# Optimization experiments

Hardware: AMD Instinct MI355X
Metric: run time of the kernel (lower is better)

## Reference

```python
import jax, jax.numpy as jnp
import numpy as np

B, N, F, T, K, FO = 16, 1024, 64, 24, 3, 64


def setup_inputs() -> dict:
    key = jax.random.key(0)
    ks = jax.random.split(key, 8)
    sc = 0.05
    x = jax.random.normal(ks[0], (B, N, F, T), dtype=jnp.float32)
    W1 = jax.random.normal(ks[1], (T,), dtype=jnp.float32) * sc
    W2 = jax.random.normal(ks[2], (F, T), dtype=jnp.float32) * sc
    W3 = jax.random.normal(ks[3], (F,), dtype=jnp.float32) * sc
    bs = jax.random.normal(ks[4], (1, N, N), dtype=jnp.float32) * sc
    Vs = jax.random.normal(ks[5], (N, N), dtype=jnp.float32) * sc
    cheb = jax.random.normal(ks[6], (K, N, N), dtype=jnp.float32) * sc
    Theta = jax.random.normal(ks[7], (K, F, FO), dtype=jnp.float32) * sc
    return {"x": x, "W1": W1, "W2": W2, "W3": W3, "bs": bs, "Vs": Vs,
            "cheb": cheb, "Theta": Theta}


def spatial_attention(x, W1, W2, W3, bs, Vs):
    # x: (B,N,F,T) -> S: (B,N,N)
    lhs = jnp.einsum('bnft,t->bnf', x, W1)          # (B,N,F)
    lhs = jnp.einsum('bnf,ft->bnt', lhs, W2)        # (B,N,T)
    rhs = jnp.einsum('f,bnft->btn', W3, x)          # (B,T,N)
    product = jnp.einsum('bnt,btm->bnm', lhs, rhs)  # (B,N,N)
    S = jnp.einsum('ik,bkj->bij', Vs, jax.nn.sigmoid(product + bs))
    return jax.nn.softmax(S, axis=1)


def reference(x, W1, W2, W3, bs, Vs, cheb, Theta):
    # x: (B,N,F,T); cheb: (K,N,N); Theta: (K,F,FO)
    S = spatial_attention(x, W1, W2, W3, bs, Vs)    # (B,N,N)
    out = jnp.zeros((x.shape[0], x.shape[1], Theta.shape[2], x.shape[3]),
                    dtype=x.dtype)
    for k in range(cheb.shape[0]):                  # small fixed K
        Tat = cheb[k] * S                           # (B,N,N) attention-masked T_k
        # T_k_with_at.permute(0,2,1) @ graph_signal, vectorized over t
        r = jnp.einsum('bnm,bnft->bmft', Tat, x)    # (B,N,F,T)
        out = out + jnp.einsum('bmft,fo->bmot', r, Theta[k])
    return jax.nn.relu(out)                         # (B,N,FO,T)
```

## Files before the change

### kernel.cpp

```cpp
#include <hip/hip_runtime.h>
#include <math.h>

#define Bc 16
#define Nc 1024
#define Fc 64
#define Tc 24
#define Kc 3
#define FOc 64
#define Cc (Fc*Tc)
#define KKc (Kc*Nc)

typedef __attribute__((ext_vector_type(8))) short short8;
typedef __attribute__((ext_vector_type(4))) float f32x4;

__device__ __forceinline__ unsigned short f2bf(float f) {
  unsigned u = __float_as_uint(f);
  u += 0x7fff + ((u >> 16) & 1);
  return (unsigned short)(u >> 16);
}
__device__ __forceinline__ float bf2f(unsigned short h) {
  return __uint_as_float((unsigned)h << 16);
}

#define GLL16(g, l) __builtin_amdgcn_global_load_lds( \
    (const __attribute__((address_space(1))) void*)(g), \
    (__attribute__((address_space(3))) void*)(l), 16, 0, 0)

__device__ __forceinline__ f32x4 mfma16(short8 a, short8 b, f32x4 c) {
  return __builtin_amdgcn_mfma_f32_16x16x32_bf16(a, b, c, 0, 0, 0);
}

__device__ __forceinline__ void gemm_core(
    const unsigned short* __restrict__ Ag, const unsigned short* __restrict__ Bg,
    int lda, int ldb, int K,
    unsigned short* As, unsigned short* Bs,
    int wave, int lane, f32x4 acc[4][4]) {
  int sr = lane >> 3;
  int sc = ((lane & 7) ^ sr) * 8;
  const unsigned short* a0 = Ag + (size_t)(wave * 32 + sr) * lda + sc;
  const unsigned short* b0 = Bg + (size_t)(wave * 32 + sr) * ldb + sc;
  unsigned short* asw = As + (wave * 32) * 64;
  unsigned short* bsw = Bs + (wave * 32) * 64;
  int rw = (wave >> 1) * 64, cw = (wave & 1) * 64;
  int frow = lane & 15;
  int q = lane >> 4;
  int p0 = (q ^ (frow & 7)) * 8;
  int p1 = ((q | 4) ^ (frow & 7)) * 8;
  for (int k0 = 0; k0 < K; k0 += 64) {
    #pragma unroll
    for (int c = 0; c < 4; ++c) {
      GLL16(a0 + (size_t)(c * 8) * lda + k0, asw + (c * 8) * 64);
      GLL16(b0 + (size_t)(c * 8) * ldb + k0, bsw + (c * 8) * 64);
    }
    __syncthreads();
    #pragma unroll
    for (int h = 0; h < 2; ++h) {
      int p = h ? p1 : p0;
      short8 afr[4], bfr[4];
      #pragma unroll
      for (int i = 0; i < 4; ++i)
        afr[i] = *(const short8*)&As[(rw + i * 16 + frow) * 64 + p];
      #pragma unroll
      for (int j = 0; j < 4; ++j)
        bfr[j] = *(const short8*)&Bs[(cw + j * 16 + frow) * 64 + p];
      #pragma unroll
      for (int i = 0; i < 4; ++i)
        #pragma unroll
        for (int j = 0; j < 4; ++j)
          acc[i][j] = mfma16(afr[i], bfr[j], acc[i][j]);
    }
    __syncthreads();
  }
}

template <int MODE, int JN>
__global__ __launch_bounds__(512) void gemm256(
    const unsigned short* __restrict__ A, const unsigned short* __restrict__ B,
    void* __restrict__ Cv, int K, int CN,
    long long Abatch, long long Bbatch, long long Cbatch) {
  __shared__ unsigned short S[2 * (256 + JN * 64) * 64];
  const int BN  = JN * 64;
  const int BUF = (256 + BN) * 64;

  int gx = gridDim.x, gy = gridDim.y;
  int nwg = gx * gy * gridDim.z;
  int bid = blockIdx.x + gx * (blockIdx.y + gy * blockIdx.z);
  int xcd = bid & 7, idx = bid >> 3;
  int qq = nwg >> 3, rr = nwg & 7;
  int lin = (xcd < rr ? xcd * (qq + 1) : rr * (qq + 1) + (xcd - rr) * qq) + idx;
  int b = lin / (gx * gy);
  int rem = lin - b * (gx * gy);
  int by = rem / gx, bx = rem - by * gx;

  int tid = threadIdx.x, wave = tid >> 6, lane = tid & 63;
  const unsigned short* Ag = A + (size_t)b * Abatch + (size_t)by * 256 * K;
  const unsigned short* Bg = B + (size_t)b * Bbatch + (size_t)bx * BN * K;

  int sr = lane >> 3;
  int sc = ((lane & 7) ^ sr) * 8;
  const unsigned short* a0 = Ag + (size_t)(wave * 32 + sr) * K + sc;
  const unsigned short* b0 = Bg + (size_t)(wave * 32 + sr) * K + sc;
  unsigned short* asw0 = S + wave * 32 * 64;
  unsigned short* bsw0 = S + 256 * 64 + wave * 32 * 64;
  unsigned short* asw1 = asw0 + BUF;
  unsigned short* bsw1 = bsw0 + BUF;

  int wm = wave >> 2, wn = wave & 3;
  int rw = wm * 128;
  int cw = wn * (JN * 16);
  int frow = lane & 15;
  int q = lane >> 4;
  int p0 = (q ^ (frow & 7)) * 8;
  int p1 = ((q | 4) ^ (frow & 7)) * 8;

  f32x4 zero = {0.f, 0.f, 0.f, 0.f};
  f32x4 acc[8][JN];
  #pragma unroll
  for (int i = 0; i < 8; ++i)
    #pragma unroll
    for (int j = 0; j < JN; ++j) acc[i][j] = zero;

  auto STAGE = [&](unsigned short* asw, unsigned short* bsw, int k0) {
    #pragma unroll
    for (int c = 0; c < 4; ++c)
      GLL16(a0 + (size_t)(c * 8) * K + k0, asw + (c * 8) * 64);
    if (wave < 2 * JN) {
      #pragma unroll
      for (int c = 0; c < 4; ++c)
        GLL16(b0 + (size_t)(c * 8) * K + k0, bsw + (c * 8) * 64);
    }
  };
  auto COMPUTE = [&](const unsigned short* As, const unsigned short* Bs) {
    #pragma unroll
    for (int h = 0; h < 2; ++h) {
      int p = h ? p1 : p0;
      short8 afr[8], bfr[JN];
      #pragma unroll
      for (int i = 0; i < 8; ++i)
        afr[i] = *(const short8*)&As[(rw + i * 16 + frow) * 64 + p];
      #pragma unroll
      for (int j = 0; j < JN; ++j)
        bfr[j] = *(const short8*)&Bs[(cw + j * 16 + frow) * 64 + p];
      #pragma unroll
      for (int i = 0; i < 8; ++i)
        #pragma unroll
        for (int j = 0; j < JN; ++j)
          acc[i][j] = mfma16(afr[i], bfr[j], acc[i][j]);
    }
  };

  STAGE(asw0, bsw0, 0);
  __syncthreads();
  int k0 = 0;
  for (;;) {
    if (k0 + 64 < K) STAGE(asw1, bsw1, k0 + 64);
    COMPUTE(S, S + 256 * 64);
    __syncthreads();
    k0 += 64;
    if (k0 >= K) break;
    if (k0 + 64 < K) STAGE(asw0, bsw0, k0 + 64);
    COMPUTE(S + BUF, S + BUF + 256 * 64);
    __syncthreads();
    k0 += 64;
    if (k0 >= K) break;
  }

  int cl = lane & 15;
  #pragma unroll
  for (int i = 0; i < 8; ++i)
    #pragma unroll
    for (int e = 0; e < 4; ++e) {
      size_t P = (size_t)by * 256 + rw + i * 16 + q * 4 + e;
      #pragma unroll
      for (int j = 0; j < JN; ++j) {
        size_t Q = (size_t)bx * BN + cw + j * 16 + cl;
        if (MODE == 0) {
          ((unsigned short*)Cv)[(size_t)b * Cbatch + P * CN + Q] = f2bf(acc[i][j][e]);
        } else {
          ((float*)Cv)[(size_t)b * Cbatch + P * CN + Q] = fmaxf(acc[i][j][e], 0.f);
        }
      }
    }
}

__global__ __launch_bounds__(256) void xprep_kernel(
    const float* __restrict__ x, const float* __restrict__ W1,
    const float* __restrict__ W2, const float* __restrict__ W3,
    unsigned short* __restrict__ xt2, unsigned short* __restrict__ lhsb,
    unsigned short* __restrict__ rhsb) {
  __shared__ float ld[4 * 1560];
  __shared__ float af[4 * 64];
  int w = threadIdx.x >> 6, lane = threadIdx.x & 63;
  size_t n = (size_t)blockIdx.x * 4 + w;
  const float* xp = x + n * Cc;
  float* lw = ld + w * 1560;
  #pragma unroll
  for (int j = 0; j < 24; ++j) {
    int i = j * 64 + lane;
    int f = i / 24, t = i - f * 24;
    lw[t * 65 + f] = xp[i];
  }
  __syncthreads();
  float a = 0.f;
  #pragma unroll
  for (int t = 0; t < Tc; ++t) a += lw[t * 65 + lane] * W1[t];
  af[w * 64 + lane] = a;
  #pragma unroll
  for (int j = 0; j < 24; ++j)
    xt2[n * Cc + j * 64 + lane] = f2bf(lw[j * 65 + lane]);
  __syncthreads();
  float l = 0.f, r = 0.f;
  if (lane < Tc) {
    #pragma unroll 8
    for (int f = 0; f < Fc; ++f) {
      l += af[w * 64 + f] * W2[f * Tc + lane];
      r += W3[f] * lw[lane * 65 + f];
    }
  }
  lhsb[n * 64 + lane] = (lane < Tc) ? f2bf(l) : (unsigned short)0;
  rhsb[n * 64 + lane] = (lane < Tc) ? f2bf(r) : (unsigned short)0;
}

__global__ __launch_bounds__(256) void misc_kernel(
    const float* __restrict__ Vs, const float* __restrict__ Theta,
    const float* __restrict__ bs, unsigned short* __restrict__ Vsbf,
    unsigned short* __restrict__ tcat, float* __restrict__ bsT) {
  __shared__ float t[64 * 65];
  int bid = blockIdx.x, tid = threadIdx.x;
  if (bid < 1024) {
    int i = (bid * 256 + tid) * 4;
    float4 v = *(const float4*)&Vs[i];
    ushort4 o;
    o.x = f2bf(v.x); o.y = f2bf(v.y); o.z = f2bf(v.z); o.w = f2bf(v.w);
    *(ushort4*)&Vsbf[i] = o;
  } else if (bid < 1088) {
    int i = (bid - 1024) * 256 + tid;
    int m2 = i >> 6, f = i & 63;
    int k = m2 >> 6, o = m2 & 63;
    tcat[i] = (m2 < 192) ? f2bf(Theta[((size_t)k * Fc + f) * FOc + o])
                         : (unsigned short)0;
  } else {
    int id = bid - 1088;
    int p0 = (id >> 4) * 64, q0 = (id & 15) * 64;
    #pragma unroll
    for (int s = 0; s < 4; ++s) {
      int qr = (tid >> 4) + s * 16, pc = (tid & 15) * 4;
      float4 v = *(const float4*)&bs[(size_t)(q0 + qr) * Nc + p0 + pc];
      t[(pc + 0) * 65 + qr] = v.x;
      t[(pc + 1) * 65 + qr] = v.y;
      t[(pc + 2) * 65 + qr] = v.z;
      t[(pc + 3) * 65 + qr] = v.w;
    }
    __syncthreads();
    #pragma unroll
    for (int s = 0; s < 4; ++s) {
      int pr = (tid >> 4) + s * 16, qc = (tid & 15) * 4;
      float4 v = {t[pr * 65 + qc], t[pr * 65 + qc + 1],
                  t[pr * 65 + qc + 2], t[pr * 65 + qc + 3]};
      *(float4*)&bsT[(size_t)(p0 + pr) * Nc + q0 + qc] = v;
    }
  }
}

__global__ __launch_bounds__(256) void chebT_kernel(
    const float* __restrict__ cheb, float* __restrict__ chebT) {
  int k = blockIdx.z;
  int n0 = blockIdx.y * 64, m0 = blockIdx.x * 64;
  __shared__ float t[64 * 65];
  const float* src = cheb + (size_t)k * Nc * Nc;
  float* dst = chebT + (size_t)k * Nc * Nc;
  int tid = threadIdx.x;
  #pragma unroll
  for (int s = 0; s < 4; ++s) {
    int nr = (tid >> 4) + s * 16, mc = (tid & 15) * 4;
    float4 v = *(const float4*)&src[(size_t)(n0 + nr) * Nc + m0 + mc];
    t[(mc + 0) * 65 + nr] = v.x;
    t[(mc + 1) * 65 + nr] = v.y;
    t[(mc + 2) * 65 + nr] = v.z;
    t[(mc + 3) * 65 + nr] = v.w;
  }
  __syncthreads();
  #pragma unroll
  for (int s = 0; s < 4; ++s) {
    int mr = (tid >> 4) + s * 16, nc = (tid & 15) * 4;
    float4 v = {t[mr * 65 + nc], t[mr * 65 + nc + 1], t[mr * 65 + nc + 2], t[mr * 65 + nc + 3]};
    *(float4*)&dst[(size_t)(m0 + mr) * Nc + n0 + nc] = v;
  }
}

__global__ __launch_bounds__(256) void masksoft_kernel(
    const float* __restrict__ chebT, const unsigned short* __restrict__ ST,
    unsigned short* __restrict__ Acat, int bbase) {
  int m  = blockIdx.x & (Nc - 1);
  int bl = blockIdx.x >> 10;
  int tid = threadIdx.x;
  const unsigned short* sp = ST + ((size_t)(bbase + bl) * Nc + m) * Nc;
  ushort4 s4 = *(const ushort4*)(sp + tid * 4);
  float v0 = bf2f(s4.x), v1 = bf2f(s4.y), v2 = bf2f(s4.z), v3 = bf2f(s4.w);
  __shared__ float redm[4], reds[4];
  int wave = tid >> 6, lane = tid & 63;
  float mx = fmaxf(fmaxf(v0, v1), fmaxf(v2, v3));
  #pragma unroll
  for (int off = 32; off; off >>= 1) mx = fmaxf(mx, __shfl_xor(mx, off));
  if (lane == 0) redm[wave] = mx;
  __syncthreads();
  mx = fmaxf(fmaxf(redm[0], redm[1]), fmaxf(redm[2], redm[3]));
  float e0 = __expf(v0 - mx), e1 = __expf(v1 - mx);
  float e2 = __expf(v2 - mx), e3 = __expf(v3 - mx);
  float sm = e0 + e1 + e2 + e3;
  #pragma unroll
  for (int off = 32; off; off >>= 1) sm += __shfl_xor(sm, off);
  if (lane == 0) reds[wave] = sm;
  __syncthreads();
  float inv = 1.f / (reds[0] + reds[1] + reds[2] + reds[3]);
  e0 *= inv; e1 *= inv; e2 *= inv; e3 *= inv;
  unsigned short* ap = Acat + ((size_t)bl * Nc + m) * KKc + tid * 4;
  #pragma unroll
  for (int k = 0; k < Kc; ++k) {
    float4 c = *(const float4*)&chebT[((size_t)k * Nc + m) * Nc + tid * 4];
    ushort4 o;
    o.x = f2bf(c.x * e0); o.y = f2bf(c.y * e1);
    o.z = f2bf(c.z * e2); o.w = f2bf(c.w * e3);
    *(ushort4*)(ap + k * Nc) = o;
  }
}

template <int MODE>
__global__ __launch_bounds__(256) void mfma_gemm_bt(
    const unsigned short* __restrict__ A, const unsigned short* __restrict__ B,
    void* __restrict__ Cv, const float* __restrict__ bias, int K, int CN,
    long long Abatch, long long Bbatch, long long Cbatch) {
  __shared__ unsigned short As[128 * 64];
  __shared__ unsigned short Bs[128 * 64];
  int gx = gridDim.x, gy = gridDim.y;
  int nwg = gx * gy * gridDim.z;
  int bid = blockIdx.x + gx * (blockIdx.y + gy * blockIdx.z);
  int xcd = bid & 7, idx = bid >> 3;
  int qq = nwg >> 3, rr = nwg & 7;
  int lin = (xcd < rr ? xcd * (qq + 1) : rr * (qq + 1) + (xcd - rr) * qq) + idx;
  int b = lin / (gx * gy);
  int rem = lin - b * (gx * gy);
  int by = rem / gx, bx = rem - by * gx;
  int tid = threadIdx.x, wave = tid >> 6, lane = tid & 63;
  const unsigned short* Ag = A + (size_t)b * Abatch + (size_t)by * 128 * K;
  const unsigned short* Bg = B + (size_t)b * Bbatch + (size_t)bx * 128 * K;
  f32x4 zero = {0.f, 0.f, 0.f, 0.f};
  f32x4 acc[4][4];
  #pragma unroll
  for (int i = 0; i < 4; ++i)
    #pragma unroll
    for (int j = 0; j < 4; ++j) acc[i][j] = zero;
  gemm_core(Ag, Bg, K, K, K, As, Bs, wave, lane, acc);
  int rw = (wave >> 1) * 64, cw = (wave & 1) * 64;
  int q = lane >> 4, cl = lane & 15;
  #pragma unroll
  for (int i = 0; i < 4; ++i)
    #pragma unroll
    for (int e = 0; e < 4; ++e) {
      size_t P = (size_t)by * 128 + rw + i * 16 + q * 4 + e;
      #pragma unroll
      for (int j = 0; j < 4; ++j) {
        size_t Q = (size_t)bx * 128 + cw + j * 16 + cl;
        if (MODE == 0) {
          ((unsigned short*)Cv)[(size_t)b * Cbatch + P * CN + Q] = f2bf(acc[i][j][e]);
        } else if (MODE == 1) {
          ((float*)Cv)[(size_t)b * Cbatch + P * CN + Q] = fmaxf(acc[i][j][e], 0.f);
        } else {
          float v = acc[i][j][e] + bias[P * CN + Q];
          ((unsigned short*)Cv)[(size_t)b * Cbatch + P * CN + Q] =
              f2bf(1.f / (1.f + __expf(-v)));
        }
      }
    }
}

__global__ __launch_bounds__(256) void y2_gemm(
    const unsigned short* __restrict__ tcat, const unsigned short* __restrict__ xt2,
    unsigned short* __restrict__ ycat, int bbase) {
  __shared__ unsigned short As[128 * 64];
  __shared__ unsigned short Bs[128 * 64];
  int z = blockIdx.z;
  int bl = z / 24, t = z - bl * 24;
  int tid = threadIdx.x, wave = tid >> 6, lane = tid & 63;
  const unsigned short* Ag = tcat + (size_t)blockIdx.y * 128 * 64;
  const unsigned short* Bg = xt2 + ((size_t)(bbase + bl) * Nc + (size_t)blockIdx.x * 128) * Cc
                             + (size_t)t * 64;
  f32x4 zero = {0.f, 0.f, 0.f, 0.f};
  f32x4 acc[4][4];
  #pragma unroll
  for (int i = 0; i < 4; ++i)
    #pragma unroll
    for (int j = 0; j < 4; ++j) acc[i][j] = zero;
  gemm_core(Ag, Bg, 64, Cc, 64, As, Bs, wave, lane, acc);
  int rw = (wave >> 1) * 64, cw = (wave & 1) * 64;
  int q = lane >> 4, cl = lane & 15;
  unsigned short* yb = ycat + (size_t)bl * Cc * KKc + (size_t)t * KKc;
  #pragma unroll
  for (int i = 0; i < 4; ++i)
    #pragma unroll
    for (int e = 0; e < 4; ++e) {
      int m2 = blockIdx.y * 128 + rw + i * 16 + q * 4 + e;
      if (m2 < 192) {
        int kk = m2 >> 6, o = m2 & 63;
        unsigned short* dst = yb + (size_t)o * 24 * KKc + kk * Nc;
        #pragma unroll
        for (int j = 0; j < 4; ++j)
          dst[blockIdx.x * 128 + cw + j * 16 + cl] = f2bf(acc[i][j][e]);
      }
    }
}

extern "C" void kernel_launch(void* const* d_in, const int* in_sizes, int n_in,
                              void* d_out, int out_size, void* d_ws, size_t ws_size,
                              hipStream_t stream) {
  const float* x     = (const float*)d_in[0];
  const float* W1    = (const float*)d_in[1];
  const float* W2    = (const float*)d_in[2];
  const float* W3    = (const float*)d_in[3];
  const float* bs    = (const float*)d_in[4];
  const float* Vs    = (const float*)d_in[5];
  const float* cheb  = (const float*)d_in[6];
  const float* Theta = (const float*)d_in[7];
  float* out = (float*)d_out;

  int passes, blcount;
  if (ws_size >= 348160000ULL) { passes = 1; blcount = 16; }
  else                         { passes = 2; blcount = 8;  }

  char* w = (char*)d_ws;
  size_t Y  = (size_t)blcount * Cc * KKc * 2;
  size_t A2 = (size_t)blcount * Nc * KKc * 2;
  unsigned short* ycat = (unsigned short*)w;
  unsigned short* Acat = (unsigned short*)(w + Y);
  unsigned short* ST   = (unsigned short*)(w + Y + A2);
  float* chebT         = (float*)(w + Y + A2 + 33554432);
  unsigned short* xt2  = (unsigned short*)(w + Y + A2 + 46137344);
  unsigned short* tcat = (unsigned short*)(w + Y + A2 + 96468992);
  unsigned short* lhsb = (unsigned short*)w;
  unsigned short* rhsb = (unsigned short*)(w + 2097152);
  unsigned short* sigT = (unsigned short*)(w + 4194304);
  float* bsT           = (float*)(w + 37748736);
  unsigned short* Vsbf = (unsigned short*)(w + 41943040);

  xprep_kernel<<<Bc * Nc / 4, 256, 0, stream>>>(x, W1, W2, W3, xt2, lhsb, rhsb);
  misc_kernel<<<1344, 256, 0, stream>>>(Vs, Theta, bs, Vsbf, tcat, bsT);
  mfma_gemm_bt<2><<<dim3(8, 8, 16), 256, 0, stream>>>(
      rhsb, lhsb, sigT, bsT, 64, Nc,
      (long long)Nc * 64, (long long)Nc * 64, (long long)Nc * Nc);
  gemm256<0, 4><<<dim3(4, 4, 16), 512, 0, stream>>>(
      sigT, Vsbf, ST, Nc, Nc,
      (long long)Nc * Nc, 0LL, (long long)Nc * Nc);
  chebT_kernel<<<dim3(16, 16, 3), 256, 0, stream>>>(cheb, chebT);

  for (int pass = 0; pass < passes; ++pass) {
    int bbase = pass * blcount;
    masksoft_kernel<<<blcount * Nc, 256, 0, stream>>>(chebT, ST, Acat, bbase);
    y2_gemm<<<dim3(Nc / 128, 2, blcount * 24), 256, 0, stream>>>(tcat, xt2, ycat, bbase);
    gemm256<1, 3><<<dim3(Cc / 192, Nc / 256, blcount), 512, 0, stream>>>(
        Acat, ycat, out + (size_t)bbase * Nc * Cc, KKc, Cc,
        (long long)Nc * KKc, (long long)Cc * KKc, (long long)Nc * Cc);
  }
}
```

Measured before the change: 577.1 us.

## Replace 256-row GEMM with 128x128 triple-buffered pipelined GEMM

```diff
diff --git a/kernel.cpp b/kernel.cpp
--- a/kernel.cpp
+++ b/kernel.cpp
@@ -73,15 +73,12 @@
   }
 }
 
-template <int MODE, int JN>
-__global__ __launch_bounds__(512) void gemm256(
+template <int MODE>
+__global__ __launch_bounds__(512) void gemm_pipe(
     const unsigned short* __restrict__ A, const unsigned short* __restrict__ B,
     void* __restrict__ Cv, int K, int CN,
     long long Abatch, long long Bbatch, long long Cbatch) {
-  __shared__ unsigned short S[2 * (256 + JN * 64) * 64];
-  const int BN  = JN * 64;
-  const int BUF = (256 + BN) * 64;
-
+  __shared__ unsigned short S[6 * 128 * 64];
   int gx = gridDim.x, gy = gridDim.y;
   int nwg = gx * gy * gridDim.z;
   int bid = blockIdx.x + gx * (blockIdx.y + gy * blockIdx.z);
@@ -93,87 +90,98 @@
   int by = rem / gx, bx = rem - by * gx;
 
   int tid = threadIdx.x, wave = tid >> 6, lane = tid & 63;
-  const unsigned short* Ag = A + (size_t)b * Abatch + (size_t)by * 256 * K;
-  const unsigned short* Bg = B + (size_t)b * Bbatch + (size_t)bx * BN * K;
+  const unsigned short* Ag = A + (size_t)b * Abatch + (size_t)by * 128 * K;
+  const unsigned short* Bg = B + (size_t)b * Bbatch + (size_t)bx * 128 * K;
 
   int sr = lane >> 3;
   int sc = ((lane & 7) ^ sr) * 8;
-  const unsigned short* a0 = Ag + (size_t)(wave * 32 + sr) * K + sc;
-  const unsigned short* b0 = Bg + (size_t)(wave * 32 + sr) * K + sc;
-  unsigned short* asw0 = S + wave * 32 * 64;
-  unsigned short* bsw0 = S + 256 * 64 + wave * 32 * 64;
-  unsigned short* asw1 = asw0 + BUF;
-  unsigned short* bsw1 = bsw0 + BUF;
+  const unsigned short* a0 = Ag + (size_t)(wave * 16 + sr) * K + sc;
+  const unsigned short* b0 = Bg + (size_t)(wave * 16 + sr) * K + sc;
+  int soff = wave * 16 * 64;
+
+  unsigned short* A0 = S;
+  unsigned short* B0 = S + 128 * 64;
+  unsigned short* A1 = S + 2 * 128 * 64;
+  unsigned short* B1 = S + 3 * 128 * 64;
+  unsigned short* A2 = S + 4 * 128 * 64;
+  unsigned short* B2 = S + 5 * 128 * 64;
 
   int wm = wave >> 2, wn = wave & 3;
-  int rw = wm * 128;
-  int cw = wn * (JN * 16);
+  int rw = wm * 64, cw = wn * 32;
   int frow = lane & 15;
   int q = lane >> 4;
   int p0 = (q ^ (frow & 7)) * 8;
   int p1 = ((q | 4) ^ (frow & 7)) * 8;
 
   f32x4 zero = {0.f, 0.f, 0.f, 0.f};
-  f32x4 acc[8][JN];
-  #pragma unroll
-  for (int i = 0; i < 8; ++i)
-    #pragma unroll
-    for (int j = 0; j < JN; ++j) acc[i][j] = zero;
-
-  auto STAGE = [&](unsigned short* asw, unsigned short* bsw, int k0) {
-    #pragma unroll
-    for (int c = 0; c < 4; ++c)
-      GLL16(a0 + (size_t)(c * 8) * K + k0, asw + (c * 8) * 64);
-    if (wave < 2 * JN) {
-      #pragma unroll
-      for (int c = 0; c < 4; ++c)
-        GLL16(b0 + (size_t)(c * 8) * K + k0, bsw + (c * 8) * 64);
-    }
+  f32x4 acc[4][2];
+  #pragma unroll
+  for (int i = 0; i < 4; ++i)
+    #pragma unroll
+    for (int j = 0; j < 2; ++j) acc[i][j] = zero;
+
+  auto STAGE = [&](unsigned short* Ab, unsigned short* Bb, int k0) {
+    GLL16(a0 + k0, Ab + soff);
+    GLL16(a0 + (size_t)8 * K + k0, Ab + soff + 8 * 64);
+    GLL16(b0 + k0, Bb + soff);
+    GLL16(b0 + (size_t)8 * K + k0, Bb + soff + 8 * 64);
   };
-  auto COMPUTE = [&](const unsigned short* As, const unsigned short* Bs) {
+  auto COMPUTE = [&](const unsigned short* As_, const unsigned short* Bs_) {
     #pragma unroll
     for (int h = 0; h < 2; ++h) {
       int p = h ? p1 : p0;
-      short8 afr[8], bfr[JN];
-      #pragma unroll
-      for (int i = 0; i < 8; ++i)
-        afr[i] = *(const short8*)&As[(rw + i * 16 + frow) * 64 + p];
-      #pragma unroll
-      for (int j = 0; j < JN; ++j)
-        bfr[j] = *(const short8*)&Bs[(cw + j * 16 + frow) * 64 + p];
-      #pragma unroll
-      for (int i = 0; i < 8; ++i)
+      short8 afr[4], bfr[2];
+      #pragma unroll
+      for (int i = 0; i < 4; ++i)
+        afr[i] = *(const short8*)&As_[(rw + i * 16 + frow) * 64 + p];
+      #pragma unroll
+      for (int j = 0; j < 2; ++j)
+        bfr[j] = *(const short8*)&Bs_[(cw + j * 16 + frow) * 64 + p];
+      __builtin_amdgcn_s_setprio(1);
+      #pragma unroll
+      for (int i = 0; i < 4; ++i)
         #pragma unroll
-        for (int j = 0; j < JN; ++j)
+        for (int j = 0; j < 2; ++j)
           acc[i][j] = mfma16(afr[i], bfr[j], acc[i][j]);
+      __builtin_amdgcn_s_setprio(0);
     }
   };
 
-  STAGE(asw0, bsw0, 0);
-  __syncthreads();
-  int k0 = 0;
-  for (;;) {
-    if (k0 + 64 < K) STAGE(asw1, bsw1, k0 + 64);
-    COMPUTE(S, S + 256 * 64);
-    __syncthreads();
-    k0 += 64;
-    if (k0 >= K) break;
-    if (k0 + 64 < K) STAGE(asw0, bsw0, k0 + 64);
-    COMPUTE(S + BUF, S + BUF + 256 * 64);
-    __syncthreads();
-    k0 += 64;
-    if (k0 >= K) break;
+  int nt = K >> 6;
+  STAGE(A0, B0, 0);
+  STAGE(A1, B1, 64);
+  asm volatile("s_waitcnt vmcnt(4)" ::: "memory");
+  __builtin_amdgcn_sched_barrier(0);
+  __builtin_amdgcn_s_barrier();
+
+  unsigned short *cA = A0, *cB = B0;
+  unsigned short *nA = A1, *nB = B1;
+  unsigned short *fA = A2, *fB = B2;
+  for (int t = 0; t < nt; ++t) {
+    if (t + 2 < nt) STAGE(fA, fB, (t + 2) << 6);
+    COMPUTE(cA, cB);
+    if (t + 1 < nt) {
+      if (t + 2 < nt) {
+        asm volatile("s_waitcnt vmcnt(4)" ::: "memory");
+      } else {
+        asm volatile("s_waitcnt vmcnt(0)" ::: "memory");
+      }
+      __builtin_amdgcn_sched_barrier(0);
+      __builtin_amdgcn_s_barrier();
+    }
+    unsigned short* tA = cA; cA = nA; nA = fA; fA = tA;
+    unsigned short* tB = cB; cB = nB; nB = fB; fB = tB;
   }
 
   int cl = lane & 15;
   #pragma unroll
-  for (int i = 0; i < 8; ++i)
+  for (int i = 0; i < 4; ++i)
     #pragma unroll
     for (int e = 0; e < 4; ++e) {
-      size_t P = (size_t)by * 256 + rw + i * 16 + q * 4 + e;
-      #pragma unroll
-      for (int j = 0; j < JN; ++j) {
-        size_t Q = (size_t)bx * BN + cw + j * 16 + cl;
+      size_t P = (size_t)by * 128 + rw + i * 16 + q * 4 + e;
+      #pragma unroll
+      for (int j = 0; j < 2; ++j) {
+        size_t Q = (size_t)bx * 128 + cw + j * 16 + cl;
         if (MODE == 0) {
           ((unsigned short*)Cv)[(size_t)b * Cbatch + P * CN + Q] = f2bf(acc[i][j][e]);
         } else {
@@ -447,7 +455,7 @@
   mfma_gemm_bt<2><<<dim3(8, 8, 16), 256, 0, stream>>>(
       rhsb, lhsb, sigT, bsT, 64, Nc,
       (long long)Nc * 64, (long long)Nc * 64, (long long)Nc * Nc);
-  gemm256<0, 4><<<dim3(4, 4, 16), 512, 0, stream>>>(
+  gemm_pipe<0><<<dim3(8, 8, 16), 512, 0, stream>>>(
       sigT, Vsbf, ST, Nc, Nc,
       (long long)Nc * Nc, 0LL, (long long)Nc * Nc);
   chebT_kernel<<<dim3(16, 16, 3), 256, 0, stream>>>(cheb, chebT);
@@ -456,7 +464,7 @@
     int bbase = pass * blcount;
     masksoft_kernel<<<blcount * Nc, 256, 0, stream>>>(chebT, ST, Acat, bbase);
     y2_gemm<<<dim3(Nc / 128, 2, blcount * 24), 256, 0, stream>>>(tcat, xt2, ycat, bbase);
-    gemm256<1, 3><<<dim3(Cc / 192, Nc / 256, blcount), 512, 0, stream>>>(
+    gemm_pipe<1><<<dim3(Cc / 128, Nc / 128, blcount), 512, 0, stream>>>(
         Acat, ycat, out + (size_t)bbase * Nc * Cc, KKc, Cc,
         (long long)Nc * KKc, (long long)Cc * KKc, (long long)Nc * Cc);
   }
```

Result: faster. 564.5 us (-2.2%).
